# Performance work log

Measured on AMD Instinct MI355X. Metric: run time of the kernel, lower is better.

## Reference

```python
import jax, jax.numpy as jnp
import numpy as np
from math import sqrt

# Complete K-ary tree: level l has K**l nodes; children of node j at level l
# are nodes j*K .. j*K+K-1 of level l+1. Levels are processed leaves->root.
K = 4
LEVELS = 9
N_NODES = (K ** LEVELS - 1) // (K - 1)  # 87381
X_SIZE = 256
H_SIZE = 256
A_SIZE = 256
N_HEADS = 8
A_K = A_SIZE // N_HEADS


def setup_inputs() -> dict:
    key = jax.random.key(0)
    ks = jax.random.split(key, 20)
    s = 0.02
    d = {
        'x': jax.random.normal(ks[0], (N_NODES, X_SIZE), dtype=jnp.float32),
        'W_iou': jax.random.normal(ks[1], (X_SIZE, 3 * H_SIZE), dtype=jnp.float32) * s,
        'b_iou': jnp.zeros((3 * H_SIZE,), dtype=jnp.float32),
        'W_f': jax.random.normal(ks[2], (X_SIZE, H_SIZE), dtype=jnp.float32) * s,
        'b_f': jnp.zeros((H_SIZE,), dtype=jnp.float32),
        'Wq': jax.random.normal(ks[3], (X_SIZE, A_SIZE), dtype=jnp.float32) * s,
        'bq': jax.random.normal(ks[4], (A_SIZE,), dtype=jnp.float32) * s,
        'Wk': jax.random.normal(ks[5], (H_SIZE, A_SIZE), dtype=jnp.float32) * s,
        'bk': jax.random.normal(ks[6], (A_SIZE,), dtype=jnp.float32) * s,
        'Wv': jax.random.normal(ks[7], (H_SIZE, A_SIZE), dtype=jnp.float32) * s,
        'bv': jax.random.normal(ks[8], (A_SIZE,), dtype=jnp.float32) * s,
        'Wl': jax.random.normal(ks[9], (A_SIZE, A_SIZE), dtype=jnp.float32) * s,
        'bl': jax.random.normal(ks[10], (A_SIZE,), dtype=jnp.float32) * s,
        'Uiou_w': jax.random.normal(ks[11], (A_SIZE, 3 * H_SIZE), dtype=jnp.float32) * s,
        'Uiou_b': jax.random.normal(ks[12], (3 * H_SIZE,), dtype=jnp.float32) * s,
        'Uf_w': jax.random.normal(ks[13], (A_SIZE, H_SIZE), dtype=jnp.float32) * s,
        'Uf_b': jax.random.normal(ks[14], (H_SIZE,), dtype=jnp.float32) * s,
    }
    return d


def _tree_lstm(x, W_iou, b_iou, W_f, b_f, Wq, bq, Wk, bk, Wv, bv, Wl, bl,
               Uiou_w, Uiou_b, Uf_w, Uf_b):
    scale = 1.0 / sqrt(A_K)
    x_iou = x @ W_iou + b_iou          # [N, 3H]
    x_f = x @ W_f + b_f                # [N, H]
    starts = [(K ** l - 1) // (K - 1) for l in range(LEVELS)]
    h_lvl = [None] * LEVELS
    c_lvl = [None] * LEVELS
    for l in reversed(range(LEVELS)):
        s0 = starts[l]
        n = K ** l
        xi = x_iou[s0:s0 + n]
        xf = x_f[s0:s0 + n]
        if l == LEVELS - 1:  # leaves: empty mailbox
            iou = xi
            fc_sum = jnp.zeros((n, H_SIZE), dtype=x.dtype)
        else:
            ch_h = h_lvl[l + 1].reshape(n, K, H_SIZE)  # children mailbox 'h'
            ch_c = c_lvl[l + 1].reshape(n, K, H_SIZE)  # children mailbox 'c'
            q = (x[s0:s0 + n] @ Wq + bq).reshape(n, N_HEADS, A_K)
            kk = (ch_h @ Wk + bk).reshape(n, K, N_HEADS, A_K)
            vv = (ch_h @ Wv + bv).reshape(n, K, N_HEADS, A_K)
            logits = jnp.einsum('nhd,nkhd->nhk', q, kk) * scale
            attn = jax.nn.softmax(logits, axis=-1)
            out = jnp.einsum('nhk,nkhd->nhd', attn, vv).reshape(n, A_SIZE)
            h_attn = out @ Wl + bl
            h_iou = h_attn @ Uiou_w + Uiou_b
            h_f = h_attn @ Uf_w + Uf_b
            f = jax.nn.sigmoid(xf + h_f)[:, None, :]   # same f for all children
            fc_sum = jnp.sum(ch_c * f, axis=1)
            iou = xi + h_iou
        i, o, u = jnp.split(iou, 3, axis=1)
        c_new = jax.nn.sigmoid(i) * jnp.tanh(u) + fc_sum
        h_new = jax.nn.sigmoid(o) * jnp.tanh(c_new)
        h_lvl[l] = h_new
        c_lvl[l] = c_new
    h = jnp.concatenate(h_lvl, axis=0)
    c = jnp.concatenate(c_lvl, axis=0)
    return h, c


def reference(x, W_iou, b_iou, W_f, b_f, Wq, bq, Wk, bk, Wv, bv, Wl, bl,
              Uiou_w, Uiou_b, Uf_w, Uf_b):
    return _tree_lstm(x, W_iou, b_iou, W_f, b_f, Wq, bq, Wk, bk, Wv, bv,
                      Wl, bl, Uiou_w, Uiou_b, Uf_w, Uf_b)
```

## Files before the change

### kernel.cpp

```cpp
#include <hip/hip_runtime.h>
#include <hip/hip_bf16.h>
#include <math.h>

constexpr int LEVELS_ = 9;
constexpr int N_NODES_ = 87381;
constexpr int HS = 256;
constexpr int N_HEADS_ = 8;

typedef __attribute__((ext_vector_type(8))) short bf16x8;
typedef __attribute__((ext_vector_type(4))) float f32x4;
typedef __attribute__((ext_vector_type(4))) float float4v;

__device__ __forceinline__ short f2bf(float f) {
    union { float f; unsigned u; } a; a.f = f;
    unsigned r = (a.u + 0x7fff + ((a.u >> 16) & 1)) >> 16;
    return (short)r;
}
__device__ __forceinline__ float bf2f(short s) {
    union { unsigned u; float f; } a; a.u = ((unsigned)(unsigned short)s) << 16;
    return a.f;
}
__device__ __forceinline__ float sigm(float x) { return 1.f / (1.f + __expf(-x)); }
__device__ __forceinline__ float ftanh(float x) {
    float e = __expf(-2.f * fabsf(x));
    float t = (1.f - e) / (1.f + e);
    return copysignf(t, x);
}

__device__ __forceinline__ void gl_lds16(const short* g, short* l) {
    __builtin_amdgcn_global_load_lds(
        (const __attribute__((address_space(1))) void*)g,
        (__attribute__((address_space(3))) void*)l, 16, 0, 0);
}

__device__ __forceinline__ int xcd_swizzle(int flat, int nwg) {
    int q = nwg >> 3, r = nwg & 7;
    int xcd = flat & 7, idx = flat >> 3;
    int base = (xcd < r) ? xcd * (q + 1) : r * (q + 1) + (xcd - r) * q;
    return base + idx;
}

__global__ __launch_bounds__(256) void gemm_bf16(
    const short* __restrict__ A, const short* __restrict__ Bt,
    const float* __restrict__ bias, const short* __restrict__ Cadd,
    void* __restrict__ Cout, int M, int N, int Kd, int out_bf16,
    short* __restrict__ Cout2, int Nsplit)
{
    __shared__ __align__(16) short smem[2 * 128 * 64];
    short* As = smem;
    short* Bs = smem + 128 * 64;

    const int tid = threadIdx.x;
    const int lane = tid & 63;
    const int w = tid >> 6;
    const int gx = gridDim.x;
    const int sw = xcd_swizzle(blockIdx.y * gx + blockIdx.x, gx * gridDim.y);
    const int row0 = (sw / gx) * 128;
    const int col0 = (sw % gx) * 128;
    const int wm = (w >> 1) * 64;
    const int wn = (w & 1) * 64;
    const int q = lane >> 4;
    const int mr = lane & 15;

    const int srl = lane >> 3;
    const int scs = ((lane & 7) ^ srl) * 8;

    f32x4 acc[4][4];
    #pragma unroll
    for (int i = 0; i < 4; i++)
        #pragma unroll
        for (int j = 0; j < 4; j++) acc[i][j] = (f32x4){0.f, 0.f, 0.f, 0.f};

    for (int k0 = 0; k0 < Kd; k0 += 64) {
        __syncthreads();
        #pragma unroll
        for (int i = 0; i < 4; ++i) {
            int s = w * 4 + i;
            int r = s * 8 + srl;
            gl_lds16(A + (size_t)(row0 + r) * Kd + k0 + scs, As + s * 512);
            gl_lds16(Bt + (size_t)(col0 + r) * Kd + k0 + scs, Bs + s * 512);
        }
        __syncthreads();
        #pragma unroll
        for (int h = 0; h < 2; ++h) {
            bf16x8 af[4], bfr[4];
            #pragma unroll
            for (int i = 0; i < 4; ++i) {
                int r = wm + i * 16 + mr;
                af[i] = *(const bf16x8*)(As + r * 64 + ((h * 4 + q) ^ (mr & 7)) * 8);
            }
            #pragma unroll
            for (int j = 0; j < 4; ++j) {
                int r = wn + j * 16 + mr;
                bfr[j] = *(const bf16x8*)(Bs + r * 64 + ((h * 4 + q) ^ (mr & 7)) * 8);
            }
            #pragma unroll
            for (int i = 0; i < 4; ++i)
                #pragma unroll
                for (int j = 0; j < 4; ++j)
                    acc[i][j] = __builtin_amdgcn_mfma_f32_16x16x32_bf16(
                        af[i], bfr[j], acc[i][j], 0, 0, 0);
        }
    }

    short* dst;
    int width, colbase;
    if (Cout2 && col0 >= Nsplit) { dst = Cout2; colbase = col0 - Nsplit; width = N - Nsplit; }
    else { dst = (short*)Cout; colbase = col0; width = Cout2 ? Nsplit : N; }

    if (out_bf16) {
        __syncthreads();
        short* Cs = smem;
        #pragma unroll
        for (int j = 0; j < 4; ++j) {
            int col = wn + j * 16 + mr;
            float bv = bias ? bias[col0 + col] : 0.f;
            #pragma unroll
            for (int i = 0; i < 4; ++i) {
                #pragma unroll
                for (int r = 0; r < 4; ++r) {
                    int lr = wm + i * 16 + q * 4 + r;
                    float v = acc[i][j][r] + bv;
                    if (Cadd && row0 + lr < M)
                        v += bf2f(Cadd[(size_t)(row0 + lr) * width + colbase + col]);
                    Cs[lr * 128 + col] = f2bf(v);
                }
            }
        }
        __syncthreads();
        #pragma unroll
        for (int i = 0; i < 8; ++i) {
            int chunk = i * 256 + tid;
            int lr = chunk >> 4;
            int c8 = (chunk & 15) * 8;
            if (row0 + lr < M)
                *(bf16x8*)(dst + (size_t)(row0 + lr) * width + colbase + c8) =
                    *(const bf16x8*)(Cs + lr * 128 + c8);
        }
    } else {
        #pragma unroll
        for (int j = 0; j < 4; ++j) {
            int col = col0 + wn + j * 16 + mr;
            float bv = bias ? bias[col] : 0.f;
            #pragma unroll
            for (int i = 0; i < 4; ++i) {
                #pragma unroll
                for (int r = 0; r < 4; ++r) {
                    int grow = row0 + wm + i * 16 + q * 4 + r;
                    if (grow < M) {
                        size_t off = (size_t)grow * N + col;
                        float v = acc[i][j][r] + bv;
                        if (Cadd) v += bf2f(Cadd[off]);
                        ((float*)Cout)[off] = v;
                    }
                }
            }
        }
    }
}

__global__ __launch_bounds__(256) void gemm_cell(
    const short* __restrict__ A, const short* __restrict__ Bt,
    const float* __restrict__ bias, const short* __restrict__ Cadd,
    const float* __restrict__ c_child,
    float* __restrict__ h_out, float* __restrict__ c_out,
    short* __restrict__ hb_out, int M)
{
    __shared__ __align__(16) short smem[128 * 136];
    short* As = smem;
    short* Bs = smem + 128 * 64;

    const int tid = threadIdx.x;
    const int lane = tid & 63;
    const int w = tid >> 6;
    const int gx = gridDim.x;
    const int sw = xcd_swizzle(blockIdx.y * gx + blockIdx.x, gx * gridDim.y);
    const int row0 = (sw / gx) * 128;
    const int bxs = sw % gx;
    const int col0 = bxs * 128;
    const int wm = (w >> 1) * 64;
    const int wn = (w & 1) * 64;
    const int q = lane >> 4;
    const int mr = lane & 15;

    const int srl = lane >> 3;
    const int scs = ((lane & 7) ^ srl) * 8;

    const bool leaf = (c_child == nullptr);
    const int jn = (leaf && wn == 64) ? 2 : 4;

    f32x4 acc[4][4];
    #pragma unroll
    for (int i = 0; i < 4; i++)
        #pragma unroll
        for (int j = 0; j < 4; j++) acc[i][j] = (f32x4){0.f, 0.f, 0.f, 0.f};

    for (int k0 = 0; k0 < 256; k0 += 64) {
        __syncthreads();
        #pragma unroll
        for (int i = 0; i < 4; ++i) {
            int s = w * 4 + i;
            int r = s * 8 + srl;
            gl_lds16(A + (size_t)(row0 + r) * 256 + k0 + scs, As + s * 512);
            if (!(leaf && s >= 12))
                gl_lds16(Bt + (size_t)(col0 + r) * 256 + k0 + scs, Bs + s * 512);
        }
        __syncthreads();
        #pragma unroll
        for (int h = 0; h < 2; ++h) {
            bf16x8 af[4], bfr[4];
            #pragma unroll
            for (int i = 0; i < 4; ++i) {
                int r = wm + i * 16 + mr;
                af[i] = *(const bf16x8*)(As + r * 64 + ((h * 4 + q) ^ (mr & 7)) * 8);
            }
            #pragma unroll
            for (int j = 0; j < 4; ++j)
                if (j < jn) {
                    int r = wn + j * 16 + mr;
                    bfr[j] = *(const bf16x8*)(Bs + r * 64 + ((h * 4 + q) ^ (mr & 7)) * 8);
                }
            #pragma unroll
            for (int i = 0; i < 4; ++i)
                #pragma unroll
                for (int j = 0; j < 4; ++j)
                    if (j < jn)
                        acc[i][j] = __builtin_amdgcn_mfma_f32_16x16x32_bf16(
                            af[i], bfr[j], acc[i][j], 0, 0, 0);
        }
    }

    __syncthreads();
    short* Cs = smem;
    #pragma unroll
    for (int j = 0; j < 4; ++j) {
        int col = wn + j * 16 + mr;
        float bv = bias[col0 + col];
        #pragma unroll
        for (int i = 0; i < 4; ++i) {
            #pragma unroll
            for (int r = 0; r < 4; ++r) {
                int lr = wm + i * 16 + q * 4 + r;
                float v = acc[i][j][r] + bv;
                if (Cadd && row0 + lr < M)
                    v += bf2f(Cadd[(size_t)(row0 + lr) * 1024 + col0 + col]);
                Cs[lr * 136 + col] = f2bf(v);
            }
        }
    }
    __syncthreads();

    const int hd0 = bxs * 32;
    #pragma unroll 1
    for (int it = 0; it < 2; ++it) {
        int chunk = it * 256 + tid;
        int row = chunk >> 2;
        int d8 = (chunk & 3) * 8;
        int gp = row0 + row;
        if (gp < M) {
            bf16x8 vi = *(const bf16x8*)(Cs + row * 136 + d8);
            bf16x8 vo = *(const bf16x8*)(Cs + row * 136 + 32 + d8);
            bf16x8 vu = *(const bf16x8*)(Cs + row * 136 + 64 + d8);
            float fc[8] = {0.f, 0.f, 0.f, 0.f, 0.f, 0.f, 0.f, 0.f};
            if (!leaf) {
                bf16x8 vf = *(const bf16x8*)(Cs + row * 136 + 96 + d8);
                #pragma unroll
                for (int c = 0; c < 4; ++c) {
                    const float* cp = c_child + (size_t)(4 * gp + c) * 256 + hd0 + d8;
                    float4v a = *(const float4v*)cp;
                    float4v b = *(const float4v*)(cp + 4);
                    #pragma unroll
                    for (int e = 0; e < 4; ++e) { fc[e] += a[e]; fc[4 + e] += b[e]; }
                }
                #pragma unroll
                for (int e = 0; e < 8; ++e) fc[e] *= sigm(bf2f(vf[e]));
            }
            float4v hv[2], cv[2];
            bf16x8 hbv;
            #pragma unroll
            for (int e = 0; e < 8; ++e) {
                float cn = sigm(bf2f(vi[e])) * ftanh(bf2f(vu[e])) + fc[e];
                float hn = sigm(bf2f(vo[e])) * ftanh(cn);
                hv[e >> 2][e & 3] = hn;
                cv[e >> 2][e & 3] = cn;
                hbv[e] = f2bf(hn);
            }
            size_t o = (size_t)gp * 256 + hd0 + d8;
            *(float4v*)(h_out + o) = hv[0]; *(float4v*)(h_out + o + 4) = hv[1];
            *(float4v*)(c_out + o) = cv[0]; *(float4v*)(c_out + o + 4) = cv[1];
            *(bf16x8*)(hb_out + o) = hbv;
        }
    }
}

__global__ __launch_bounds__(256) void kv_attn(
    const short* __restrict__ A,
    const short* __restrict__ B3t,
    const float* __restrict__ bias_kv,
    const short* __restrict__ qb_lvl,
    short* __restrict__ outb)
{
    __shared__ __align__(16) short smem[2 * 128 * 64 + 32 * 64];
    short* As = smem;
    short* Bs = smem + 128 * 64;
    short* sh_o = smem + 2 * 128 * 64;

    const int tid = threadIdx.x;
    const int lane = tid & 63;
    const int w = tid >> 6;
    const int gx = gridDim.x;
    const int sw = xcd_swizzle(blockIdx.y * gx + blockIdx.x, gx * gridDim.y);
    const int byq = sw / gx;
    const int colb = sw % gx;
    const int row0 = byq * 128;
    const int col0 = colb * 128;
    const int wm = (w >> 1) * 64;
    const int wn = (w & 1) * 64;
    const int q = lane >> 4;
    const int mr = lane & 15;

    const int srl = lane >> 3;
    const int scs = ((lane & 7) ^ srl) * 8;

    f32x4 acc[4][4];
    #pragma unroll
    for (int i = 0; i < 4; i++)
        #pragma unroll
        for (int j = 0; j < 4; j++) acc[i][j] = (f32x4){0.f, 0.f, 0.f, 0.f};

    for (int k0 = 0; k0 < 256; k0 += 64) {
        __syncthreads();
        #pragma unroll
        for (int i = 0; i < 4; ++i) {
            int s = w * 4 + i;
            int r = s * 8 + srl;
            gl_lds16(A + (size_t)(row0 + r) * 256 + k0 + scs, As + s * 512);
            gl_lds16(B3t + (size_t)(col0 + r) * 256 + k0 + scs, Bs + s * 512);
        }
        __syncthreads();
        #pragma unroll
        for (int h = 0; h < 2; ++h) {
            bf16x8 af[4], bfr[4];
            #pragma unroll
            for (int i = 0; i < 4; ++i) {
                int r = wm + i * 16 + mr;
                af[i] = *(const bf16x8*)(As + r * 64 + ((h * 4 + q) ^ (mr & 7)) * 8);
            }
            #pragma unroll
            for (int j = 0; j < 4; ++j) {
                int r = wn + j * 16 + mr;
                bfr[j] = *(const bf16x8*)(Bs + r * 64 + ((h * 4 + q) ^ (mr & 7)) * 8);
            }
            #pragma unroll
            for (int i = 0; i < 4; ++i)
                #pragma unroll
                for (int j = 0; j < 4; ++j)
                    acc[i][j] = __builtin_amdgcn_mfma_f32_16x16x32_bf16(
                        af[i], bfr[j], acc[i][j], 0, 0, 0);
        }
    }

    __syncthreads();
    short* Cs = smem;
    #pragma unroll
    for (int j = 0; j < 4; ++j) {
        int col = wn + j * 16 + mr;
        float bv = bias_kv[col0 + col];
        #pragma unroll
        for (int i = 0; i < 4; ++i) {
            #pragma unroll
            for (int r = 0; r < 4; ++r) {
                int lr = wm + i * 16 + q * 4 + r;
                Cs[lr * 128 + col] = f2bf(acc[i][j][r] + bv);
            }
        }
    }
    __syncthreads();

    const int p0 = byq * 32;
    const int grp0 = tid >> 5;
    const int l32 = tid & 31;
    #pragma unroll 1
    for (int it = 0; it < 8; ++it) {
        int pair = it * 8 + grp0;
        int pl = pair >> 1, hh = pair & 1;
        float qv = bf2f(qb_lvl[(size_t)(p0 + pl) * 256 + (colb * 2 + hh) * 32 + l32]);
        float logit[4];
        #pragma unroll
        for (int c = 0; c < 4; ++c) {
            float pch = qv * bf2f(Cs[(4 * pl + c) * 128 + hh * 64 + l32]);
            #pragma unroll
            for (int off = 16; off >= 1; off >>= 1)
                pch += __shfl_xor(pch, off, 32);
            logit[c] = pch * 0.17677669529663687f;
        }
        float mx = fmaxf(fmaxf(logit[0], logit[1]), fmaxf(logit[2], logit[3]));
        float e[4], s = 0.f;
        #pragma unroll
        for (int c = 0; c < 4; ++c) { e[c] = __expf(logit[c] - mx); s += e[c]; }
        float inv = 1.f / s;
        float o = 0.f;
        #pragma unroll
        for (int c = 0; c < 4; ++c)
            o += (e[c] * inv) * bf2f(Cs[(4 * pl + c) * 128 + hh * 64 + 32 + l32]);
        sh_o[pl * 64 + hh * 32 + l32] = f2bf(o);
    }
    __syncthreads();
    {
        int r = tid >> 3, c8 = (tid & 7) * 8;
        *(bf16x8*)(outb + (size_t)(p0 + r) * 256 + colb * 64 + c8) =
            *(const bf16x8*)(sh_o + r * 64 + c8);
    }
}

__global__ __launch_bounds__(256) void level_fused(
    const short* __restrict__ hb, const float* __restrict__ c_all,
    const short* __restrict__ qb, const short* __restrict__ xi,
    const short* __restrict__ B3t, const short* __restrict__ Wlt,
    const short* __restrict__ Bt2,
    const float* __restrict__ bias_kv, const float* __restrict__ bl,
    const float* __restrict__ biasU,
    float* __restrict__ h_all, float* __restrict__ c_out_g,
    short* __restrict__ hb_out, int s0, int sc, int n)
{
    __shared__ __align__(16) char smem[50176];
    short* sh_h    = (short*)smem;
    short* sh_kv   = (short*)(smem + 16896);
    short* sh_out  = (short*)smem;
    short* sh_ha   = (short*)(smem + 8448);
    float* sh_iouf = (float*)(smem + 16896);

    const int tid = threadIdx.x;
    const int lane = tid & 63;
    const int w = tid >> 6;
    const int q = lane >> 4;
    const int mr = lane & 15;
    const int p0 = blockIdx.x * 8;
    const int np = (n - p0 < 8) ? (n - p0) : 8;
    const int nch = 4 * np;

    #pragma unroll
    for (int i = 0; i < 4; ++i) {
        int chunk = i * 256 + tid;
        int r = chunk >> 5;
        int c8 = (chunk & 31) * 8;
        bf16x8 v = {};
        if (r < nch) v = *(const bf16x8*)(hb + (size_t)(sc + 4 * p0 + r) * 256 + c8);
        *(bf16x8*)(sh_h + r * 264 + c8) = v;
    }
    __syncthreads();

    {
        f32x4 acc[2][8];
        #pragma unroll
        for (int rt = 0; rt < 2; ++rt)
            #pragma unroll
            for (int ct = 0; ct < 8; ++ct) acc[rt][ct] = (f32x4){0.f, 0.f, 0.f, 0.f};
        #pragma unroll 1
        for (int k0 = 0; k0 < 256; k0 += 32) {
            bf16x8 a0 = *(const bf16x8*)(sh_h + mr * 264 + k0 + q * 8);
            bf16x8 a1 = *(const bf16x8*)(sh_h + (16 + mr) * 264 + k0 + q * 8);
            #pragma unroll
            for (int ct = 0; ct < 8; ++ct) {
                int col = w * 128 + ct * 16 + mr;
                bf16x8 b = *(const bf16x8*)(B3t + (size_t)col * 256 + k0 + q * 8);
                acc[0][ct] = __builtin_amdgcn_mfma_f32_16x16x32_bf16(a0, b, acc[0][ct], 0, 0, 0);
                acc[1][ct] = __builtin_amdgcn_mfma_f32_16x16x32_bf16(a1, b, acc[1][ct], 0, 0, 0);
            }
        }
        #pragma unroll
        for (int ct = 0; ct < 8; ++ct) {
            int col = w * 128 + ct * 16 + mr;
            float bv = bias_kv[col];
            #pragma unroll
            for (int rt = 0; rt < 2; ++rt)
                #pragma unroll
                for (int r = 0; r < 4; ++r) {
                    int row = rt * 16 + q * 4 + r;
                    sh_kv[row * 520 + col] = f2bf(acc[rt][ct][r] + bv);
                }
        }
    }
    __syncthreads();

    {
        const int grp0 = tid >> 5;
        const int l32 = tid & 31;
        #pragma unroll 1
        for (int it = 0; it < 8; ++it) {
            int grp = it * 8 + grp0;
            int node = grp >> 3, head = grp & 7;
            if (node < np) {
                float qv = bf2f(qb[(size_t)(s0 + p0 + node) * 256 + head * 32 + l32]);
                float logit[4];
                #pragma unroll
                for (int c = 0; c < 4; ++c) {
                    float p = qv * bf2f(sh_kv[(4 * node + c) * 520 + head * 64 + l32]);
                    #pragma unroll
                    for (int off = 16; off >= 1; off >>= 1)
                        p += __shfl_xor(p, off, 32);
                    logit[c] = p * 0.17677669529663687f;
                }
                float mx = fmaxf(fmaxf(logit[0], logit[1]), fmaxf(logit[2], logit[3]));
                float e[4], s = 0.f;
                #pragma unroll
                for (int c = 0; c < 4; ++c) { e[c] = __expf(logit[c] - mx); s += e[c]; }
                float inv = 1.f / s;
                float o = 0.f;
                #pragma unroll
                for (int c = 0; c < 4; ++c)
                    o += (e[c] * inv) * bf2f(sh_kv[(4 * node + c) * 520 + head * 64 + 32 + l32]);
                sh_out[node * 264 + head * 32 + l32] = f2bf(o);
            }
        }
    }
    __syncthreads();

    {
        f32x4 acc[4];
        #pragma unroll
        for (int ct = 0; ct < 4; ++ct) acc[ct] = (f32x4){0.f, 0.f, 0.f, 0.f};
        #pragma unroll 1
        for (int k0 = 0; k0 < 256; k0 += 32) {
            bf16x8 a = *(const bf16x8*)(sh_out + mr * 264 + k0 + q * 8);
            #pragma unroll
            for (int ct = 0; ct < 4; ++ct) {
                int col = w * 64 + ct * 16 + mr;
                bf16x8 b = *(const bf16x8*)(Wlt + (size_t)col * 256 + k0 + q * 8);
                acc[ct] = __builtin_amdgcn_mfma_f32_16x16x32_bf16(a, b, acc[ct], 0, 0, 0);
            }
        }
        #pragma unroll
        for (int ct = 0; ct < 4; ++ct) {
            int col = w * 64 + ct * 16 + mr;
            float bv = bl[col];
            #pragma unroll
            for (int r = 0; r < 4; ++r) {
                int row = q * 4 + r;
                if (row < np) sh_ha[row * 264 + col] = f2bf(acc[ct][r] + bv);
            }
        }
    }
    __syncthreads();

    {
        f32x4 acc[16];
        #pragma unroll
        for (int ct = 0; ct < 16; ++ct) acc[ct] = (f32x4){0.f, 0.f, 0.f, 0.f};
        #pragma unroll 1
        for (int k0 = 0; k0 < 256; k0 += 32) {
            bf16x8 a = *(const bf16x8*)(sh_ha + mr * 264 + k0 + q * 8);
            #pragma unroll
            for (int ct = 0; ct < 16; ++ct) {
                int col = w * 256 + ct * 16 + mr;
                bf16x8 b = *(const bf16x8*)(Bt2 + (size_t)col * 256 + k0 + q * 8);
                acc[ct] = __builtin_amdgcn_mfma_f32_16x16x32_bf16(a, b, acc[ct], 0, 0, 0);
            }
        }
        __syncthreads();
        #pragma unroll
        for (int ct = 0; ct < 16; ++ct) {
            int col = w * 256 + ct * 16 + mr;
            float bU = biasU[col];
            #pragma unroll
            for (int r = 0; r < 4; ++r) {
                int row = q * 4 + r;
                if (row < np)
                    sh_iouf[row * 1024 + col] =
                        acc[ct][r] + bU + bf2f(xi[(size_t)(s0 + p0 + row) * 1024 + col]);
            }
        }
    }
    __syncthreads();

    #pragma unroll 1
    for (int it = 0; it < 8; ++it) {
        int t = it * 256 + tid;
        if (t < np * 256) {
            int node = t >> 8, j = t & 255;
            int gcol = (j >> 5) * 128 + (j & 31);
            float iv = sh_iouf[node * 1024 + gcol];
            float ov = sh_iouf[node * 1024 + gcol + 32];
            float uv = sh_iouf[node * 1024 + gcol + 64];
            float fv = sigm(sh_iouf[node * 1024 + gcol + 96]);
            float fc = 0.f;
            #pragma unroll
            for (int c = 0; c < 4; ++c)
                fc += c_all[(size_t)(sc + 4 * (p0 + node) + c) * 256 + j] * fv;
            float cn = sigm(iv) * ftanh(uv) + fc;
            float hn = sigm(ov) * ftanh(cn);
            size_t o = (size_t)(s0 + p0 + node) * 256 + j;
            h_all[o] = hn;
            c_out_g[o] = cn;
            hb_out[o] = f2bf(hn);
        }
    }
}

__global__ __launch_bounds__(256) void conv_x(
    const float* __restrict__ x, short* __restrict__ xb, int n8)
{
    int t = blockIdx.x * 256 + threadIdx.x;
    if (t >= n8) return;
    float4v a = *(const float4v*)(x + (size_t)t * 8);
    float4v b = *(const float4v*)(x + (size_t)t * 8 + 4);
    bf16x8 o;
    o[0] = f2bf(a.x); o[1] = f2bf(a.y); o[2] = f2bf(a.z); o[3] = f2bf(a.w);
    o[4] = f2bf(b.x); o[5] = f2bf(b.y); o[6] = f2bf(b.z); o[7] = f2bf(b.w);
    *(bf16x8*)(xb + (size_t)t * 8) = o;
}

__global__ __launch_bounds__(256) void prep_weights(
    const float* __restrict__ W_iou, const float* __restrict__ W_f,
    const float* __restrict__ Uiou_w, const float* __restrict__ Uf_w,
    const float* __restrict__ Wk, const float* __restrict__ Wv,
    const float* __restrict__ Wq, const float* __restrict__ Wl,
    const float* __restrict__ b_iou, const float* __restrict__ b_f,
    const float* __restrict__ Uiou_b, const float* __restrict__ Uf_b,
    const float* __restrict__ bk, const float* __restrict__ bv,
    const float* __restrict__ bq,
    short* __restrict__ Bt1, short* __restrict__ Bt2, short* __restrict__ B3t,
    short* __restrict__ Wqt, short* __restrict__ Wlt,
    float* __restrict__ biasX, float* __restrict__ biasU,
    float* __restrict__ bias_kv)
{
    int t = blockIdx.x * 256 + threadIdx.x;
    if (t < 262144) {
        int gc = t >> 8, k = t & 255;
        int within = gc & 127, gate = within >> 5, d = (gc >> 7) * 32 + (within & 31);
        float v = (gate < 3) ? W_iou[k * 768 + gate * 256 + d] : W_f[k * 256 + d];
        Bt1[t] = f2bf(v);
        return;
    }
    t -= 262144;
    if (t < 262144) {
        int gc = t >> 8, k = t & 255;
        int within = gc & 127, gate = within >> 5, d = (gc >> 7) * 32 + (within & 31);
        float v = (gate < 3) ? Uiou_w[k * 768 + gate * 256 + d] : Uf_w[k * 256 + d];
        Bt2[t] = f2bf(v);
        return;
    }
    t -= 262144;
    if (t < 131072) {
        int gc = t >> 8, k = t & 255;
        int head = gc >> 6, kv = (gc >> 5) & 1, d = head * 32 + (gc & 31);
        float v = kv ? Wv[k * 256 + d] : Wk[k * 256 + d];
        B3t[t] = f2bf(v);
        return;
    }
    t -= 131072;
    if (t < 65536) { int nn = t >> 8, k = t & 255; Wqt[t] = f2bf(Wq[k * 256 + nn]); return; }
    t -= 65536;
    if (t < 65536) { int nn = t >> 8, k = t & 255; Wlt[t] = f2bf(Wl[k * 256 + nn]); return; }
    t -= 65536;
    if (t < 1024) {
        int within = t & 127, gate = within >> 5, d = (t >> 7) * 32 + (within & 31);
        biasX[t] = (gate < 3) ? b_iou[gate * 256 + d] : b_f[d];
        return;
    }
    t -= 1024;
    if (t < 256) { biasX[1024 + t] = bq[t]; return; }
    t -= 256;
    if (t < 1024) {
        int within = t & 127, gate = within >> 5, d = (t >> 7) * 32 + (within & 31);
        biasU[t] = (gate < 3) ? Uiou_b[gate * 256 + d] : Uf_b[d];
        return;
    }
    t -= 1024;
    if (t < 512) {
        int head = t >> 6, kv = (t >> 5) & 1, d = head * 32 + (t & 31);
        bias_kv[t] = kv ? bv[d] : bk[d];
        return;
    }
}

static inline void launch_gemm(const short* A, const short* Bt, const float* bias,
                               const short* Cadd, void* C, int M, int N, int Kd,
                               int out_bf16, short* C2, int Nsplit, hipStream_t stream)
{
    dim3 grid(N / 128, (M + 127) / 128);
    gemm_bf16<<<grid, 256, 0, stream>>>(A, Bt, bias, Cadd, C, M, N, Kd, out_bf16,
                                        C2, Nsplit);
}

extern "C" void kernel_launch(void* const* d_in, const int* in_sizes, int n_in,
                              void* d_out, int out_size, void* d_ws, size_t ws_size,
                              hipStream_t stream)
{
    const float* x      = (const float*)d_in[0];
    const float* W_iou  = (const float*)d_in[1];
    const float* b_iou  = (const float*)d_in[2];
    const float* W_f    = (const float*)d_in[3];
    const float* b_f    = (const float*)d_in[4];
    const float* Wq     = (const float*)d_in[5];
    const float* bq     = (const float*)d_in[6];
    const float* Wk     = (const float*)d_in[7];
    const float* bk     = (const float*)d_in[8];
    const float* Wv     = (const float*)d_in[9];
    const float* bv     = (const float*)d_in[10];
    const float* Wl     = (const float*)d_in[11];
    const float* bl     = (const float*)d_in[12];
    const float* Uiou_w = (const float*)d_in[13];
    const float* Uiou_b = (const float*)d_in[14];
    const float* Uf_w   = (const float*)d_in[15];
    const float* Uf_b   = (const float*)d_in[16];

    float* h_all = (float*)d_out;
    float* c_all = h_all + (size_t)N_NODES_ * HS;

    char* p = (char*)d_ws;
    short* xb   = (short*)p; p += (size_t)N_NODES_ * 256 * 2;
    short* hb   = (short*)p; p += (size_t)N_NODES_ * 256 * 2;
    short* xi   = (short*)p; p += (size_t)21845 * 1024 * 2;
    short* qb   = (short*)p; p += (size_t)21845 * 256 * 2;
    short* outb = (short*)p; p += (size_t)16384 * 256 * 2;
    short* hab  = (short*)p; p += (size_t)16384 * 256 * 2;
    short* Bt1  = (short*)p; p += (size_t)1024 * 256 * 2;
    short* Wqt  = (short*)p; p += (size_t)256 * 256 * 2;
    short* Bt2  = (short*)p; p += (size_t)1024 * 256 * 2;
    short* B3t  = (short*)p; p += (size_t)512 * 256 * 2;
    short* Wlt  = (short*)p; p += (size_t)256 * 256 * 2;
    float* biasX   = (float*)p; p += 1280 * 4;
    float* biasU   = (float*)p; p += 1024 * 4;
    float* bias_kv = (float*)p; p += 512 * 4;

    static const int starts[LEVELS_] = {0, 1, 5, 21, 85, 341, 1365, 5461, 21845};

    {
        int n8 = N_NODES_ * 256 / 8;
        conv_x<<<(n8 + 255) / 256, 256, 0, stream>>>(x, xb, n8);
        int total = 262144 + 262144 + 131072 + 65536 + 65536 + 1024 + 256 + 1024 + 512;
        prep_weights<<<(total + 255) / 256, 256, 0, stream>>>(
            W_iou, W_f, Uiou_w, Uf_w, Wk, Wv, Wq, Wl,
            b_iou, b_f, Uiou_b, Uf_b, bk, bv, bq,
            Bt1, Bt2, B3t, Wqt, Wlt, biasX, biasU, bias_kv);
    }

    launch_gemm(xb, Bt1, biasX, nullptr, xi, 21845, 1280, 256, 1, qb, 1024, stream);

    {
        dim3 grid(8, 65536 / 128);
        gemm_cell<<<grid, 256, 0, stream>>>(
            xb + (size_t)21845 * 256, Bt1, biasX, nullptr, nullptr,
            h_all + (size_t)21845 * HS, c_all + (size_t)21845 * HS,
            hb + (size_t)21845 * HS, 65536);
    }

    for (int l = 7; l >= 6; l--) {
        int n  = 1 << (2 * l);
        int s0 = starts[l];
        int sc = starts[l + 1];
        int nc = 4 * n;

        dim3 gkv(4, nc / 128);
        kv_attn<<<gkv, 256, 0, stream>>>(
            hb + (size_t)sc * 256, B3t, bias_kv, qb + (size_t)s0 * 256, outb);
        launch_gemm(outb, Wlt, bl, nullptr, hab, n, 256, 256, 1, nullptr, 0, stream);
        dim3 gc(8, n / 128);
        gemm_cell<<<gc, 256, 0, stream>>>(
            hab, Bt2, biasU, xi + (size_t)s0 * 1024, c_all + (size_t)sc * HS,
            h_all + (size_t)s0 * HS, c_all + (size_t)s0 * HS,
            hb + (size_t)s0 * HS, n);
    }

    for (int l = 5; l >= 0; l--) {
        int n  = 1 << (2 * l);
        int s0 = starts[l];
        int sc = starts[l + 1];
        int blocks = (n + 7) / 8;
        level_fused<<<blocks, 256, 0, stream>>>(
            hb, c_all, qb, xi, B3t, Wlt, Bt2, bias_kv, bl, biasU,
            h_all, c_all, hb, s0, sc, n);
    }
}
```

Baseline: 848.9 us.

## Double-buffer GEMM LDS tiles and merge upper tree levels into one persistent kernel

The GEMM, cell and kv_attn kernels now use two LDS buffers, so the next K-tile is prefetched while MFMAs run on the current one. This removes one barrier per K step, but doubles shared memory per block, which may reduce occupancy. The six per-level launches for levels 5..0 become a single 128-block kernel that loops over levels, separated by atomic grid barriers whose counters are zeroed in prep_weights. This removes launch overhead for the tiny top levels. It relies on all 128 blocks being co-resident, and blocks spin-wait at each barrier.

```diff
diff --git a/kernel.cpp b/kernel.cpp
--- a/kernel.cpp
+++ b/kernel.cpp
@@ -38,6 +38,17 @@
     int xcd = flat & 7, idx = flat >> 3;
     int base = (xcd < r) ? xcd * (q + 1) : r * (q + 1) + (xcd - r) * q;
     return base + idx;
+}
+
+__device__ __forceinline__ void gridbar(int* c, int nb) {
+    __syncthreads();
+    if (threadIdx.x == 0) {
+        __threadfence();
+        atomicAdd(c, 1);
+        while (atomicAdd(c, 0) < nb) __builtin_amdgcn_s_sleep(2);
+        __threadfence();
+    }
+    __syncthreads();
 }
 
 __global__ __launch_bounds__(256) void gemm_bf16(
@@ -46,9 +57,7 @@
     void* __restrict__ Cout, int M, int N, int Kd, int out_bf16,
     short* __restrict__ Cout2, int Nsplit)
 {
-    __shared__ __align__(16) short smem[2 * 128 * 64];
-    short* As = smem;
-    short* Bs = smem + 128 * 64;
+    __shared__ __align__(16) short smem[32768];
 
     const int tid = threadIdx.x;
     const int lane = tid & 63;
@@ -65,14 +74,9 @@
     const int srl = lane >> 3;
     const int scs = ((lane & 7) ^ srl) * 8;
 
-    f32x4 acc[4][4];
-    #pragma unroll
-    for (int i = 0; i < 4; i++)
-        #pragma unroll
-        for (int j = 0; j < 4; j++) acc[i][j] = (f32x4){0.f, 0.f, 0.f, 0.f};
-
-    for (int k0 = 0; k0 < Kd; k0 += 64) {
-        __syncthreads();
+    auto stage = [&](int b, int k0) {
+        short* As = smem + b * 16384;
+        short* Bs = As + 8192;
         #pragma unroll
         for (int i = 0; i < 4; ++i) {
             int s = w * 4 + i;
@@ -80,7 +84,21 @@
             gl_lds16(A + (size_t)(row0 + r) * Kd + k0 + scs, As + s * 512);
             gl_lds16(Bt + (size_t)(col0 + r) * Kd + k0 + scs, Bs + s * 512);
         }
-        __syncthreads();
+    };
+
+    f32x4 acc[4][4];
+    #pragma unroll
+    for (int i = 0; i < 4; i++)
+        #pragma unroll
+        for (int j = 0; j < 4; j++) acc[i][j] = (f32x4){0.f, 0.f, 0.f, 0.f};
+
+    stage(0, 0);
+    __syncthreads();
+    const int nk = Kd >> 6;
+    for (int t = 0; t < nk; ++t) {
+        if (t + 1 < nk) stage((t + 1) & 1, (t + 1) << 6);
+        const short* As = smem + (t & 1) * 16384;
+        const short* Bs = As + 8192;
         #pragma unroll
         for (int h = 0; h < 2; ++h) {
             bf16x8 af[4], bfr[4];
@@ -101,6 +119,7 @@
                     acc[i][j] = __builtin_amdgcn_mfma_f32_16x16x32_bf16(
                         af[i], bfr[j], acc[i][j], 0, 0, 0);
         }
+        __syncthreads();
     }
 
     short* dst;
@@ -109,7 +128,6 @@
     else { dst = (short*)Cout; colbase = col0; width = Cout2 ? Nsplit : N; }
 
     if (out_bf16) {
-        __syncthreads();
         short* Cs = smem;
         #pragma unroll
         for (int j = 0; j < 4; ++j) {
@@ -166,9 +184,7 @@
     float* __restrict__ h_out, float* __restrict__ c_out,
     short* __restrict__ hb_out, int M)
 {
-    __shared__ __align__(16) short smem[128 * 136];
-    short* As = smem;
-    short* Bs = smem + 128 * 64;
+    __shared__ __align__(16) short smem[32768];
 
     const int tid = threadIdx.x;
     const int lane = tid & 63;
@@ -189,14 +205,9 @@
     const bool leaf = (c_child == nullptr);
     const int jn = (leaf && wn == 64) ? 2 : 4;
 
-    f32x4 acc[4][4];
-    #pragma unroll
-    for (int i = 0; i < 4; i++)
-        #pragma unroll
-        for (int j = 0; j < 4; j++) acc[i][j] = (f32x4){0.f, 0.f, 0.f, 0.f};
-
-    for (int k0 = 0; k0 < 256; k0 += 64) {
-        __syncthreads();
+    auto stage = [&](int b, int k0) {
+        short* As = smem + b * 16384;
+        short* Bs = As + 8192;
         #pragma unroll
         for (int i = 0; i < 4; ++i) {
             int s = w * 4 + i;
@@ -205,7 +216,20 @@
             if (!(leaf && s >= 12))
                 gl_lds16(Bt + (size_t)(col0 + r) * 256 + k0 + scs, Bs + s * 512);
         }
-        __syncthreads();
+    };
+
+    f32x4 acc[4][4];
+    #pragma unroll
+    for (int i = 0; i < 4; i++)
+        #pragma unroll
+        for (int j = 0; j < 4; j++) acc[i][j] = (f32x4){0.f, 0.f, 0.f, 0.f};
+
+    stage(0, 0);
+    __syncthreads();
+    for (int t = 0; t < 4; ++t) {
+        if (t + 1 < 4) stage((t + 1) & 1, (t + 1) << 6);
+        const short* As = smem + (t & 1) * 16384;
+        const short* Bs = As + 8192;
         #pragma unroll
         for (int h = 0; h < 2; ++h) {
             bf16x8 af[4], bfr[4];
@@ -228,9 +252,9 @@
                         acc[i][j] = __builtin_amdgcn_mfma_f32_16x16x32_bf16(
                             af[i], bfr[j], acc[i][j], 0, 0, 0);
         }
-    }
-
-    __syncthreads();
+        __syncthreads();
+    }
+
     short* Cs = smem;
     #pragma unroll
     for (int j = 0; j < 4; ++j) {
@@ -300,10 +324,8 @@
     const short* __restrict__ qb_lvl,
     short* __restrict__ outb)
 {
-    __shared__ __align__(16) short smem[2 * 128 * 64 + 32 * 64];
-    short* As = smem;
-    short* Bs = smem + 128 * 64;
-    short* sh_o = smem + 2 * 128 * 64;
+    __shared__ __align__(16) short smem[32768 + 2048];
+    short* sh_o = smem + 32768;
 
     const int tid = threadIdx.x;
     const int lane = tid & 63;
@@ -322,14 +344,9 @@
     const int srl = lane >> 3;
     const int scs = ((lane & 7) ^ srl) * 8;
 
-    f32x4 acc[4][4];
-    #pragma unroll
-    for (int i = 0; i < 4; i++)
-        #pragma unroll
-        for (int j = 0; j < 4; j++) acc[i][j] = (f32x4){0.f, 0.f, 0.f, 0.f};
-
-    for (int k0 = 0; k0 < 256; k0 += 64) {
-        __syncthreads();
+    auto stage = [&](int b, int k0) {
+        short* As = smem + b * 16384;
+        short* Bs = As + 8192;
         #pragma unroll
         for (int i = 0; i < 4; ++i) {
             int s = w * 4 + i;
@@ -337,7 +354,20 @@
             gl_lds16(A + (size_t)(row0 + r) * 256 + k0 + scs, As + s * 512);
             gl_lds16(B3t + (size_t)(col0 + r) * 256 + k0 + scs, Bs + s * 512);
         }
-        __syncthreads();
+    };
+
+    f32x4 acc[4][4];
+    #pragma unroll
+    for (int i = 0; i < 4; i++)
+        #pragma unroll
+        for (int j = 0; j < 4; j++) acc[i][j] = (f32x4){0.f, 0.f, 0.f, 0.f};
+
+    stage(0, 0);
+    __syncthreads();
+    for (int t = 0; t < 4; ++t) {
+        if (t + 1 < 4) stage((t + 1) & 1, (t + 1) << 6);
+        const short* As = smem + (t & 1) * 16384;
+        const short* Bs = As + 8192;
         #pragma unroll
         for (int h = 0; h < 2; ++h) {
             bf16x8 af[4], bfr[4];
@@ -358,9 +388,9 @@
                     acc[i][j] = __builtin_amdgcn_mfma_f32_16x16x32_bf16(
                         af[i], bfr[j], acc[i][j], 0, 0, 0);
         }
-    }
-
-    __syncthreads();
+        __syncthreads();
+    }
+
     short* Cs = smem;
     #pragma unroll
     for (int j = 0; j < 4; ++j) {
@@ -413,15 +443,14 @@
     }
 }
 
-__global__ __launch_bounds__(256) void level_fused(
-    const short* __restrict__ hb, const float* __restrict__ c_all,
+__global__ __launch_bounds__(256) void level_fused_all(
+    short* hb, float* c_all,
     const short* __restrict__ qb, const short* __restrict__ xi,
     const short* __restrict__ B3t, const short* __restrict__ Wlt,
     const short* __restrict__ Bt2,
     const float* __restrict__ bias_kv, const float* __restrict__ bl,
     const float* __restrict__ biasU,
-    float* __restrict__ h_all, float* __restrict__ c_out_g,
-    short* __restrict__ hb_out, int s0, int sc, int n)
+    float* h_all, int* bar)
 {
     __shared__ __align__(16) char smem[50176];
     short* sh_h    = (short*)smem;
@@ -435,165 +464,176 @@
     const int w = tid >> 6;
     const int q = lane >> 4;
     const int mr = lane & 15;
-    const int p0 = blockIdx.x * 8;
-    const int np = (n - p0 < 8) ? (n - p0) : 8;
-    const int nch = 4 * np;
-
-    #pragma unroll
-    for (int i = 0; i < 4; ++i) {
-        int chunk = i * 256 + tid;
-        int r = chunk >> 5;
-        int c8 = (chunk & 31) * 8;
-        bf16x8 v = {};
-        if (r < nch) v = *(const bf16x8*)(hb + (size_t)(sc + 4 * p0 + r) * 256 + c8);
-        *(bf16x8*)(sh_h + r * 264 + c8) = v;
-    }
-    __syncthreads();
-
-    {
-        f32x4 acc[2][8];
-        #pragma unroll
-        for (int rt = 0; rt < 2; ++rt)
-            #pragma unroll
-            for (int ct = 0; ct < 8; ++ct) acc[rt][ct] = (f32x4){0.f, 0.f, 0.f, 0.f};
-        #pragma unroll 1
-        for (int k0 = 0; k0 < 256; k0 += 32) {
-            bf16x8 a0 = *(const bf16x8*)(sh_h + mr * 264 + k0 + q * 8);
-            bf16x8 a1 = *(const bf16x8*)(sh_h + (16 + mr) * 264 + k0 + q * 8);
-            #pragma unroll
-            for (int ct = 0; ct < 8; ++ct) {
-                int col = w * 128 + ct * 16 + mr;
-                bf16x8 b = *(const bf16x8*)(B3t + (size_t)col * 256 + k0 + q * 8);
-                acc[0][ct] = __builtin_amdgcn_mfma_f32_16x16x32_bf16(a0, b, acc[0][ct], 0, 0, 0);
-                acc[1][ct] = __builtin_amdgcn_mfma_f32_16x16x32_bf16(a1, b, acc[1][ct], 0, 0, 0);
-            }
-        }
-        #pragma unroll
-        for (int ct = 0; ct < 8; ++ct) {
-            int col = w * 128 + ct * 16 + mr;
-            float bv = bias_kv[col];
-            #pragma unroll
-            for (int rt = 0; rt < 2; ++rt)
-                #pragma unroll
-                for (int r = 0; r < 4; ++r) {
-                    int row = rt * 16 + q * 4 + r;
-                    sh_kv[row * 520 + col] = f2bf(acc[rt][ct][r] + bv);
-                }
-        }
-    }
-    __syncthreads();
-
-    {
-        const int grp0 = tid >> 5;
-        const int l32 = tid & 31;
-        #pragma unroll 1
-        for (int it = 0; it < 8; ++it) {
-            int grp = it * 8 + grp0;
-            int node = grp >> 3, head = grp & 7;
-            if (node < np) {
-                float qv = bf2f(qb[(size_t)(s0 + p0 + node) * 256 + head * 32 + l32]);
-                float logit[4];
-                #pragma unroll
-                for (int c = 0; c < 4; ++c) {
-                    float p = qv * bf2f(sh_kv[(4 * node + c) * 520 + head * 64 + l32]);
+
+    static constexpr int st[7] = {0, 1, 5, 21, 85, 341, 1365};
+
+    for (int l = 5; l >= 0; --l) {
+        const int n  = 1 << (2 * l);
+        const int s0 = st[l];
+        const int sc = st[l + 1];
+        const int p0 = blockIdx.x * 8;
+        if (p0 < n) {
+            const int np = (n - p0 < 8) ? (n - p0) : 8;
+            const int nch = 4 * np;
+
+            #pragma unroll
+            for (int i = 0; i < 4; ++i) {
+                int chunk = i * 256 + tid;
+                int r = chunk >> 5;
+                int c8 = (chunk & 31) * 8;
+                bf16x8 v = {};
+                if (r < nch) v = *(const bf16x8*)(hb + (size_t)(sc + 4 * p0 + r) * 256 + c8);
+                *(bf16x8*)(sh_h + r * 264 + c8) = v;
+            }
+            __syncthreads();
+
+            {
+                f32x4 acc[2][8];
+                #pragma unroll
+                for (int rt = 0; rt < 2; ++rt)
                     #pragma unroll
-                    for (int off = 16; off >= 1; off >>= 1)
-                        p += __shfl_xor(p, off, 32);
-                    logit[c] = p * 0.17677669529663687f;
-                }
-                float mx = fmaxf(fmaxf(logit[0], logit[1]), fmaxf(logit[2], logit[3]));
-                float e[4], s = 0.f;
-                #pragma unroll
-                for (int c = 0; c < 4; ++c) { e[c] = __expf(logit[c] - mx); s += e[c]; }
-                float inv = 1.f / s;
-                float o = 0.f;
-                #pragma unroll
-                for (int c = 0; c < 4; ++c)
-                    o += (e[c] * inv) * bf2f(sh_kv[(4 * node + c) * 520 + head * 64 + 32 + l32]);
-                sh_out[node * 264 + head * 32 + l32] = f2bf(o);
-            }
-        }
-    }
-    __syncthreads();
-
-    {
-        f32x4 acc[4];
-        #pragma unroll
-        for (int ct = 0; ct < 4; ++ct) acc[ct] = (f32x4){0.f, 0.f, 0.f, 0.f};
-        #pragma unroll 1
-        for (int k0 = 0; k0 < 256; k0 += 32) {
-            bf16x8 a = *(const bf16x8*)(sh_out + mr * 264 + k0 + q * 8);
-            #pragma unroll
-            for (int ct = 0; ct < 4; ++ct) {
-                int col = w * 64 + ct * 16 + mr;
-                bf16x8 b = *(const bf16x8*)(Wlt + (size_t)col * 256 + k0 + q * 8);
-                acc[ct] = __builtin_amdgcn_mfma_f32_16x16x32_bf16(a, b, acc[ct], 0, 0, 0);
-            }
-        }
-        #pragma unroll
-        for (int ct = 0; ct < 4; ++ct) {
-            int col = w * 64 + ct * 16 + mr;
-            float bv = bl[col];
-            #pragma unroll
-            for (int r = 0; r < 4; ++r) {
-                int row = q * 4 + r;
-                if (row < np) sh_ha[row * 264 + col] = f2bf(acc[ct][r] + bv);
-            }
-        }
-    }
-    __syncthreads();
-
-    {
-        f32x4 acc[16];
-        #pragma unroll
-        for (int ct = 0; ct < 16; ++ct) acc[ct] = (f32x4){0.f, 0.f, 0.f, 0.f};
-        #pragma unroll 1
-        for (int k0 = 0; k0 < 256; k0 += 32) {
-            bf16x8 a = *(const bf16x8*)(sh_ha + mr * 264 + k0 + q * 8);
-            #pragma unroll
-            for (int ct = 0; ct < 16; ++ct) {
-                int col = w * 256 + ct * 16 + mr;
-                bf16x8 b = *(const bf16x8*)(Bt2 + (size_t)col * 256 + k0 + q * 8);
-                acc[ct] = __builtin_amdgcn_mfma_f32_16x16x32_bf16(a, b, acc[ct], 0, 0, 0);
-            }
-        }
-        __syncthreads();
-        #pragma unroll
-        for (int ct = 0; ct < 16; ++ct) {
-            int col = w * 256 + ct * 16 + mr;
-            float bU = biasU[col];
-            #pragma unroll
-            for (int r = 0; r < 4; ++r) {
-                int row = q * 4 + r;
-                if (row < np)
-                    sh_iouf[row * 1024 + col] =
-                        acc[ct][r] + bU + bf2f(xi[(size_t)(s0 + p0 + row) * 1024 + col]);
-            }
-        }
-    }
-    __syncthreads();
-
-    #pragma unroll 1
-    for (int it = 0; it < 8; ++it) {
-        int t = it * 256 + tid;
-        if (t < np * 256) {
-            int node = t >> 8, j = t & 255;
-            int gcol = (j >> 5) * 128 + (j & 31);
-            float iv = sh_iouf[node * 1024 + gcol];
-            float ov = sh_iouf[node * 1024 + gcol + 32];
-            float uv = sh_iouf[node * 1024 + gcol + 64];
-            float fv = sigm(sh_iouf[node * 1024 + gcol + 96]);
-            float fc = 0.f;
-            #pragma unroll
-            for (int c = 0; c < 4; ++c)
-                fc += c_all[(size_t)(sc + 4 * (p0 + node) + c) * 256 + j] * fv;
-            float cn = sigm(iv) * ftanh(uv) + fc;
-            float hn = sigm(ov) * ftanh(cn);
-            size_t o = (size_t)(s0 + p0 + node) * 256 + j;
-            h_all[o] = hn;
-            c_out_g[o] = cn;
-            hb_out[o] = f2bf(hn);
-        }
+                    for (int ct = 0; ct < 8; ++ct) acc[rt][ct] = (f32x4){0.f, 0.f, 0.f, 0.f};
+                #pragma unroll 1
+                for (int k0 = 0; k0 < 256; k0 += 32) {
+                    bf16x8 a0 = *(const bf16x8*)(sh_h + mr * 264 + k0 + q * 8);
+                    bf16x8 a1 = *(const bf16x8*)(sh_h + (16 + mr) * 264 + k0 + q * 8);
+                    #pragma unroll
+                    for (int ct = 0; ct < 8; ++ct) {
+                        int col = w * 128 + ct * 16 + mr;
+                        bf16x8 b = *(const bf16x8*)(B3t + (size_t)col * 256 + k0 + q * 8);
+                        acc[0][ct] = __builtin_amdgcn_mfma_f32_16x16x32_bf16(a0, b, acc[0][ct], 0, 0, 0);
+                        acc[1][ct] = __builtin_amdgcn_mfma_f32_16x16x32_bf16(a1, b, acc[1][ct], 0, 0, 0);
+                    }
+                }
+                #pragma unroll
+                for (int ct = 0; ct < 8; ++ct) {
+                    int col = w * 128 + ct * 16 + mr;
+                    float bv = bias_kv[col];
+                    #pragma unroll
+                    for (int rt = 0; rt < 2; ++rt)
+                        #pragma unroll
+                        for (int r = 0; r < 4; ++r) {
+                            int row = rt * 16 + q * 4 + r;
+                            sh_kv[row * 520 + col] = f2bf(acc[rt][ct][r] + bv);
+                        }
+                }
+            }
+            __syncthreads();
+
+            {
+                const int grp0 = tid >> 5;
+                const int l32 = tid & 31;
+                #pragma unroll 1
+                for (int it = 0; it < 8; ++it) {
+                    int grp = it * 8 + grp0;
+                    int node = grp >> 3, head = grp & 7;
+                    if (node < np) {
+                        float qv = bf2f(qb[(size_t)(s0 + p0 + node) * 256 + head * 32 + l32]);
+                        float logit[4];
+                        #pragma unroll
+                        for (int c = 0; c < 4; ++c) {
+                            float p = qv * bf2f(sh_kv[(4 * node + c) * 520 + head * 64 + l32]);
+                            #pragma unroll
+                            for (int off = 16; off >= 1; off >>= 1)
+                                p += __shfl_xor(p, off, 32);
+                            logit[c] = p * 0.17677669529663687f;
+                        }
+                        float mx = fmaxf(fmaxf(logit[0], logit[1]), fmaxf(logit[2], logit[3]));
+                        float e[4], s = 0.f;
+                        #pragma unroll
+                        for (int c = 0; c < 4; ++c) { e[c] = __expf(logit[c] - mx); s += e[c]; }
+                        float inv = 1.f / s;
+                        float o = 0.f;
+                        #pragma unroll
+                        for (int c = 0; c < 4; ++c)
+                            o += (e[c] * inv) * bf2f(sh_kv[(4 * node + c) * 520 + head * 64 + 32 + l32]);
+                        sh_out[node * 264 + head * 32 + l32] = f2bf(o);
+                    }
+                }
+            }
+            __syncthreads();
+
+            {
+                f32x4 acc[4];
+                #pragma unroll
+                for (int ct = 0; ct < 4; ++ct) acc[ct] = (f32x4){0.f, 0.f, 0.f, 0.f};
+                #pragma unroll 1
+                for (int k0 = 0; k0 < 256; k0 += 32) {
+                    bf16x8 a = *(const bf16x8*)(sh_out + mr * 264 + k0 + q * 8);
+                    #pragma unroll
+                    for (int ct = 0; ct < 4; ++ct) {
+                        int col = w * 64 + ct * 16 + mr;
+                        bf16x8 b = *(const bf16x8*)(Wlt + (size_t)col * 256 + k0 + q * 8);
+                        acc[ct] = __builtin_amdgcn_mfma_f32_16x16x32_bf16(a, b, acc[ct], 0, 0, 0);
+                    }
+                }
+                #pragma unroll
+                for (int ct = 0; ct < 4; ++ct) {
+                    int col = w * 64 + ct * 16 + mr;
+                    float bv = bl[col];
+                    #pragma unroll
+                    for (int r = 0; r < 4; ++r) {
+                        int row = q * 4 + r;
+                        if (row < np) sh_ha[row * 264 + col] = f2bf(acc[ct][r] + bv);
+                    }
+                }
+            }
+            __syncthreads();
+
+            {
+                f32x4 acc[16];
+                #pragma unroll
+                for (int ct = 0; ct < 16; ++ct) acc[ct] = (f32x4){0.f, 0.f, 0.f, 0.f};
+                #pragma unroll 1
+                for (int k0 = 0; k0 < 256; k0 += 32) {
+                    bf16x8 a = *(const bf16x8*)(sh_ha + mr * 264 + k0 + q * 8);
+                    #pragma unroll
+                    for (int ct = 0; ct < 16; ++ct) {
+                        int col = w * 256 + ct * 16 + mr;
+                        bf16x8 b = *(const bf16x8*)(Bt2 + (size_t)col * 256 + k0 + q * 8);
+                        acc[ct] = __builtin_amdgcn_mfma_f32_16x16x32_bf16(a, b, acc[ct], 0, 0, 0);
+                    }
+                }
+                __syncthreads();
+                #pragma unroll
+                for (int ct = 0; ct < 16; ++ct) {
+                    int col = w * 256 + ct * 16 + mr;
+                    float bU = biasU[col];
+                    #pragma unroll
+                    for (int r = 0; r < 4; ++r) {
+                        int row = q * 4 + r;
+                        if (row < np)
+                            sh_iouf[row * 1024 + col] =
+                                acc[ct][r] + bU + bf2f(xi[(size_t)(s0 + p0 + row) * 1024 + col]);
+                    }
+                }
+            }
+            __syncthreads();
+
+            #pragma unroll 1
+            for (int it = 0; it < 8; ++it) {
+                int t = it * 256 + tid;
+                if (t < np * 256) {
+                    int node = t >> 8, j = t & 255;
+                    int gcol = (j >> 5) * 128 + (j & 31);
+                    float iv = sh_iouf[node * 1024 + gcol];
+                    float ov = sh_iouf[node * 1024 + gcol + 32];
+                    float uv = sh_iouf[node * 1024 + gcol + 64];
+                    float fv = sigm(sh_iouf[node * 1024 + gcol + 96]);
+                    float fc = 0.f;
+                    #pragma unroll
+                    for (int c = 0; c < 4; ++c)
+                        fc += c_all[(size_t)(sc + 4 * (p0 + node) + c) * 256 + j] * fv;
+                    float cn = sigm(iv) * ftanh(uv) + fc;
+                    float hn = sigm(ov) * ftanh(cn);
+                    size_t o = (size_t)(s0 + p0 + node) * 256 + j;
+                    h_all[o] = hn;
+                    c_all[o] = cn;
+                    hb[o] = f2bf(hn);
+                }
+            }
+        }
+        if (l > 0) gridbar(bar + (5 - l), gridDim.x);
     }
 }
 
@@ -622,7 +662,7 @@
     short* __restrict__ Bt1, short* __restrict__ Bt2, short* __restrict__ B3t,
     short* __restrict__ Wqt, short* __restrict__ Wlt,
     float* __restrict__ biasX, float* __restrict__ biasU,
-    float* __restrict__ bias_kv)
+    float* __restrict__ bias_kv, int* __restrict__ bar)
 {
     int t = blockIdx.x * 256 + threadIdx.x;
     if (t < 262144) {
@@ -672,6 +712,8 @@
         bias_kv[t] = kv ? bv[d] : bk[d];
         return;
     }
+    t -= 512;
+    if (t < 8) { bar[t] = 0; return; }
 }
 
 static inline void launch_gemm(const short* A, const short* Bt, const float* bias,
@@ -723,17 +765,18 @@
     float* biasX   = (float*)p; p += 1280 * 4;
     float* biasU   = (float*)p; p += 1024 * 4;
     float* bias_kv = (float*)p; p += 512 * 4;
+    int*   bar     = (int*)p;   p += 8 * 4;
 
     static const int starts[LEVELS_] = {0, 1, 5, 21, 85, 341, 1365, 5461, 21845};
 
     {
         int n8 = N_NODES_ * 256 / 8;
         conv_x<<<(n8 + 255) / 256, 256, 0, stream>>>(x, xb, n8);
-        int total = 262144 + 262144 + 131072 + 65536 + 65536 + 1024 + 256 + 1024 + 512;
+        int total = 262144 + 262144 + 131072 + 65536 + 65536 + 1024 + 256 + 1024 + 512 + 8;
         prep_weights<<<(total + 255) / 256, 256, 0, stream>>>(
             W_iou, W_f, Uiou_w, Uf_w, Wk, Wv, Wq, Wl,
             b_iou, b_f, Uiou_b, Uf_b, bk, bv, bq,
-            Bt1, Bt2, B3t, Wqt, Wlt, biasX, biasU, bias_kv);
+            Bt1, Bt2, B3t, Wqt, Wlt, biasX, biasU, bias_kv, bar);
     }
 
     launch_gemm(xb, Bt1, biasX, nullptr, xi, 21845, 1280, 256, 1, qb, 1024, stream);
@@ -763,13 +806,6 @@
             hb + (size_t)s0 * HS, n);
     }
 
-    for (int l = 5; l >= 0; l--) {
-        int n  = 1 << (2 * l);
-        int s0 = starts[l];
-        int sc = starts[l + 1];
-        int blocks = (n + 7) / 8;
-        level_fused<<<blocks, 256, 0, stream>>>(
-            hb, c_all, qb, xi, B3t, Wlt, Bt2, bias_kv, bl, biasU,
-            h_all, c_all, hb, s0, sc, n);
-    }
-}
+    level_fused_all<<<128, 256, 0, stream>>>(
+        hb, c_all, qb, xi, B3t, Wlt, Bt2, bias_kv, bl, biasU, h_all, bar);
+}
```

After: 877.5 us. 3.4% more time.
